# Optimization experiments

Measured on AMD Instinct MI355X. Metric: run time of the kernel, lower is better.

Reference implementation:

```python
import jax, jax.numpy as jnp
import numpy as np

B, T, D, H = 128, 1024, 256, 256


def setup_inputs() -> dict:
    key = jax.random.key(0)
    k1, k2, k3 = jax.random.split(key, 3)
    x = jax.random.normal(k1, (B, T, D), dtype=jnp.float32)
    # flax LSTMCell: input projections (no bias), hidden projections (with bias)
    Wi = jax.random.normal(k2, (D, 4 * H), dtype=jnp.float32) * (1.0 / np.sqrt(D))
    Wh = jax.random.normal(k3, (H, 4 * H), dtype=jnp.float32) * (1.0 / np.sqrt(H))
    bh = jnp.zeros((4 * H,), dtype=jnp.float32)
    return {"x": x, "Wi": Wi, "Wh": Wh, "bh": bh}


def reference(x, Wi, Wh, bh):
    # Unrolled LSTM over time with zero-initialized carry; dropout is identity
    # (deterministic, training=False).
    b, t, d = x.shape
    h_dim = Wh.shape[0]
    # Precompute all input-side gate projections: [B, T, 4H]
    xg = jnp.einsum("btd,dg->btg", x, Wi)

    def step(carry, xg_t):
        c, h = carry
        gates = xg_t + h @ Wh + bh  # [B, 4H]
        i, f, g, o = jnp.split(gates, 4, axis=-1)
        i = jax.nn.sigmoid(i)
        f = jax.nn.sigmoid(f)
        g = jnp.tanh(g)
        o = jax.nn.sigmoid(o)
        c_new = f * c + i * g
        h_new = o * jnp.tanh(c_new)
        return (c_new, h_new), h_new

    c0 = jnp.zeros((b, h_dim), dtype=x.dtype)
    h0 = jnp.zeros((b, h_dim), dtype=x.dtype)
    (c_fin, h_fin), ys = jax.lax.scan(step, (c0, h0), jnp.swapaxes(xg, 0, 1))
    outputs = jnp.swapaxes(ys, 0, 1)  # [B, T, H]
    return outputs, c_fin, h_fin
```

## Files before the change

kernel.cpp:

```cpp
#include <hip/hip_runtime.h>
#include <hip/hip_bf16.h>
#include <stdint.h>

typedef unsigned short u16;
typedef short short8 __attribute__((ext_vector_type(8)));
typedef float floatx4 __attribute__((ext_vector_type(4)));
typedef float f32x4 __attribute__((ext_vector_type(4)));

__device__ __forceinline__ u16 f2bf(float f) {
  union { float f; uint32_t u; } v; v.f = f;
  return (u16)((v.u + 0x7FFFu + ((v.u >> 16) & 1u)) >> 16);
}
__device__ __forceinline__ float fexp(float x) {
  return __builtin_amdgcn_exp2f(x * 1.44269504088896340736f);
}
__device__ __forceinline__ float sigm(float x) {
  return __builtin_amdgcn_rcpf(1.0f + fexp(-x));
}
__device__ __forceinline__ float tanh_(float x) {
  return 1.0f - 2.0f * __builtin_amdgcn_rcpf(1.0f + fexp(2.0f * x));
}
__device__ __forceinline__ uint32_t packbf(float hi, float lo) {
  union { float f; uint32_t u; } a, b; a.f = hi; b.f = lo;
  return __builtin_amdgcn_perm(a.u + 0x8000u, b.u + 0x8000u, 0x07060302u);
}

__device__ __forceinline__ short8 ld_b128_mall(const void* p) {
  short8 v;
  asm volatile("global_load_dwordx4 %0, %1, off sc0 sc1"
               : "=v"(v) : "v"(p) : "memory");
  return v;
}
__device__ __forceinline__ short8 ld_b128_xcd(const void* p) {
  short8 v;
  asm volatile("global_load_dwordx4 %0, %1, off sc0"
               : "=v"(v) : "v"(p) : "memory");
  return v;
}
__device__ __forceinline__ uint32_t ld_b32_mall_wait(const void* p) {
  uint32_t v;
  asm volatile("global_load_dword %0, %1, off sc0 sc1\n\ts_waitcnt vmcnt(0)"
               : "=v"(v) : "v"(p) : "memory");
  return v;
}
__device__ __forceinline__ uint32_t ld_b32_xcd_wait(const void* p) {
  uint32_t v;
  asm volatile("global_load_dword %0, %1, off sc0\n\ts_waitcnt vmcnt(0)"
               : "=v"(v) : "v"(p) : "memory");
  return v;
}
__device__ __forceinline__ void st_b16_mall(void* p, uint32_t v) {
  asm volatile("global_store_short %0, %1, off sc0 sc1"
               :: "v"(p), "v"(v) : "memory");
}
__device__ __forceinline__ void st_b32_mall(void* p, uint32_t v) {
  asm volatile("global_store_dword %0, %1, off sc0 sc1"
               :: "v"(p), "v"(v) : "memory");
}

__global__ void k1_prep(const float* __restrict__ Wi, const float* __restrict__ Wh,
                        u16* __restrict__ Wi_t, u16* __restrict__ Wh_t) {
  const int idx = blockIdx.x * 256 + threadIdx.x;
  const int n = idx >> 8, k = idx & 255;
  Wi_t[idx] = f2bf(Wi[k * 1024 + n]);
  Wh_t[idx] = f2bf(Wh[k * 1024 + n]);
}

template <bool FAST>
__device__ __forceinline__ void lstm_scan(
    const u16* __restrict__ Wi_t, const u16* __restrict__ Wh_t,
    const float* __restrict__ x, const float* __restrict__ bh,
    u16* __restrict__ h_ring, uint32_t* __restrict__ flags,
    float* __restrict__ out, int g, int j, int l) {
  const int lq = l >> 4, ln = l & 15;
  const int colBase = j * 16 + ln;

  short8 bfI[4][8], bfW[4][8];
#pragma unroll
  for (int gp = 0; gp < 4; ++gp)
#pragma unroll
    for (int kk = 0; kk < 8; ++kk) {
      const size_t o = (size_t)(gp * 256 + colBase) * 256 + kk * 32 + lq * 8;
      bfI[gp][kk] = *(const short8*)(Wi_t + o);
      bfW[gp][kk] = *(const short8*)(Wh_t + o);
    }
  float bias[4];
#pragma unroll
  for (int gp = 0; gp < 4; ++gp) bias[gp] = bh[gp * 256 + colBase];

  floatx4 xga[4];
  {
    f32x4 xf[16];
    const float* xp = x + (size_t)(g * 16 + ln) * 262144 + lq * 8;
#pragma unroll
    for (int kk = 0; kk < 8; ++kk) {
      xf[2 * kk]     = *(const f32x4*)(xp + kk * 32);
      xf[2 * kk + 1] = *(const f32x4*)(xp + kk * 32 + 4);
    }
#pragma unroll
    for (int gp = 0; gp < 4; ++gp)
      xga[gp] = (floatx4){bias[gp], bias[gp], bias[gp], bias[gp]};
#pragma unroll
    for (int kk = 0; kk < 8; ++kk) {
      union { uint32_t u[4]; short8 s; } cv;
      cv.u[0] = packbf(xf[2 * kk][1], xf[2 * kk][0]);
      cv.u[1] = packbf(xf[2 * kk][3], xf[2 * kk][2]);
      cv.u[2] = packbf(xf[2 * kk + 1][1], xf[2 * kk + 1][0]);
      cv.u[3] = packbf(xf[2 * kk + 1][3], xf[2 * kk + 1][2]);
#pragma unroll
      for (int gp = 0; gp < 4; ++gp)
        xga[gp] = __builtin_amdgcn_mfma_f32_16x16x32_bf16(cv.s, bfI[gp][kk],
                                                          xga[gp], 0, 0, 0);
    }
  }

  float creg[4] = {0.f, 0.f, 0.f, 0.f};
  float hv[4]   = {0.f, 0.f, 0.f, 0.f};

  for (int t = 0; t < 1024; ++t) {
    if (t > 0) {
      const uint32_t* fp = flags + (((g << 2) | (t & 3)) << 4) + (l & 15);
      if (FAST) { while (!__all(ld_b32_xcd_wait(fp)  == (uint32_t)t)) {} }
      else      { while (!__all(ld_b32_mall_wait(fp) == (uint32_t)t)) {} }
    }
    const u16* hs = h_ring + (size_t)(t & 3) * 32768 + g * 4096;
    short8 af[8];
#pragma unroll
    for (int kk = 0; kk < 8; ++kk) {
      const u16* ap = hs + ln * 256 + kk * 32 + lq * 8;
      af[kk] = FAST ? ld_b128_xcd(ap) : ld_b128_mall(ap);
    }
    f32x4 xf[16];
    if (t < 1023) {
      const float* xp = x + (size_t)(g * 16 + ln) * 262144 + (size_t)(t + 1) * 256 + lq * 8;
#pragma unroll
      for (int kk = 0; kk < 8; ++kk) {
        xf[2 * kk]     = *(const f32x4*)(xp + kk * 32);
        xf[2 * kk + 1] = *(const f32x4*)(xp + kk * 32 + 4);
      }
      asm volatile("s_waitcnt vmcnt(16)" ::: "memory");
    } else {
      asm volatile("s_waitcnt vmcnt(0)" ::: "memory");
    }
    __builtin_amdgcn_sched_barrier(0);
    floatx4 acc[4];
#pragma unroll
    for (int gp = 0; gp < 4; ++gp) acc[gp] = xga[gp];
#pragma unroll
    for (int kk = 0; kk < 8; ++kk)
#pragma unroll
      for (int gp = 0; gp < 4; ++gp)
        acc[gp] = __builtin_amdgcn_mfma_f32_16x16x32_bf16(af[kk], bfW[gp][kk],
                                                          acc[gp], 0, 0, 0);
#pragma unroll
    for (int r = 0; r < 4; ++r) {
      const float iv = sigm(acc[0][r]);
      const float fv = sigm(acc[1][r]);
      const float gv = tanh_(acc[2][r]);
      const float ov = sigm(acc[3][r]);
      const float cc = fv * creg[r] + iv * gv;
      creg[r] = cc;
      hv[r] = ov * tanh_(cc);
    }
    u16* hd = h_ring + (size_t)((t + 1) & 3) * 32768 + g * 4096;
#pragma unroll
    for (int r = 0; r < 4; ++r) {
      if (FAST) hd[(lq * 4 + r) * 256 + colBase] = f2bf(hv[r]);
      else st_b16_mall(hd + (lq * 4 + r) * 256 + colBase, (uint32_t)f2bf(hv[r]));
    }
    asm volatile("s_waitcnt vmcnt(0)" ::: "memory");
    if (l == 0) {
      uint32_t* fp = flags + (((g << 2) | ((t + 1) & 3)) << 4) + j;
      if (FAST) *fp = (uint32_t)(t + 1);
      else st_b32_mall(fp, (uint32_t)(t + 1));
    }
#pragma unroll
    for (int r = 0; r < 4; ++r) {
      float* yp = out + ((size_t)(g * 16 + lq * 4 + r) * 1024 + t) * 256 + colBase;
      if (FAST) *yp = hv[r];
      else __builtin_nontemporal_store(hv[r], yp);
    }
    if (t < 1023) {
#pragma unroll
      for (int gp = 0; gp < 4; ++gp)
        xga[gp] = (floatx4){bias[gp], bias[gp], bias[gp], bias[gp]};
#pragma unroll
      for (int kk = 0; kk < 8; ++kk) {
        union { uint32_t u[4]; short8 s; } cv;
        cv.u[0] = packbf(xf[2 * kk][1], xf[2 * kk][0]);
        cv.u[1] = packbf(xf[2 * kk][3], xf[2 * kk][2]);
        cv.u[2] = packbf(xf[2 * kk + 1][1], xf[2 * kk + 1][0]);
        cv.u[3] = packbf(xf[2 * kk + 1][3], xf[2 * kk + 1][2]);
#pragma unroll
        for (int gp = 0; gp < 4; ++gp)
          xga[gp] = __builtin_amdgcn_mfma_f32_16x16x32_bf16(cv.s, bfI[gp][kk],
                                                            xga[gp], 0, 0, 0);
      }
    }
  }
#pragma unroll
  for (int r = 0; r < 4; ++r) {
    const int b = g * 16 + lq * 4 + r;
    out[33554432 + b * 256 + colBase] = creg[r];
    out[33554432 + 32768 + b * 256 + colBase] = hv[r];
  }
}

__global__ __launch_bounds__(64, 1) void k3_lstm(
    const u16* __restrict__ Wi_t, const u16* __restrict__ Wh_t,
    const float* __restrict__ x, const float* __restrict__ bh,
    u16* __restrict__ h_ring, uint32_t* __restrict__ flags,
    uint32_t* __restrict__ xcc_arr, float* __restrict__ out) {
  const int g = blockIdx.x & 7;
  const int j = blockIdx.x >> 3;
  const int l = threadIdx.x;

  uint32_t xcc;
  asm volatile("s_getreg_b32 %0, hwreg(HW_REG_XCC_ID)" : "=s"(xcc));
  if (l == 0) st_b32_mall(xcc_arr + blockIdx.x, xcc + 1u);
  const uint32_t* xp_ = xcc_arr + g + 8 * (l & 15);
  uint32_t peer;
  do { peer = ld_b32_mall_wait(xp_); } while (!__all(peer != 0u));
  const bool fast = (bool)__all(peer == __builtin_amdgcn_readfirstlane(peer));

  if (fast) lstm_scan<true >(Wi_t, Wh_t, x, bh, h_ring, flags, out, g, j, l);
  else      lstm_scan<false>(Wi_t, Wh_t, x, bh, h_ring, flags, out, g, j, l);
}

extern "C" void kernel_launch(void* const* d_in, const int* in_sizes, int n_in,
                              void* d_out, int out_size, void* d_ws, size_t ws_size,
                              hipStream_t stream) {
  const float* x  = (const float*)d_in[0];
  const float* Wi = (const float*)d_in[1];
  const float* Wh = (const float*)d_in[2];
  const float* bh = (const float*)d_in[3];
  char* ws = (char*)d_ws;
  u16* Wi_t         = (u16*)(ws);
  u16* Wh_t         = (u16*)(ws + 524288);
  uint32_t* flags   = (uint32_t*)(ws + 1048576);
  uint32_t* xcc_arr = (uint32_t*)(ws + 1048576 + 2048);
  u16* h_ring       = (u16*)(ws + 1052672);
  float* out = (float*)d_out;

  hipMemsetAsync(ws + 1048576, 0, 4096, stream);
  hipMemsetAsync(h_ring, 0, 4 * 65536, stream);
  k1_prep<<<dim3(1024), dim3(256), 0, stream>>>(Wi, Wh, Wi_t, Wh_t);
  k3_lstm<<<dim3(128), dim3(64), 0, stream>>>(Wi_t, Wh_t, x, bh, h_ring, flags,
                                              xcc_arr, out);
}
```

Before: 2.603 ms.

## Prefetch x two steps ahead and pad flags to separate cache lines

The x loads for step t+2 are now issued after the current step's input projection is packed, so each load has a whole recurrence step to land. This lets the per-step wait become a full vmcnt(0) without stalling on fresh x loads. Each per-block sync flag is also padded to its own 64-byte slot, meant to stop false sharing and contention between the 16 flags polled per group. The flag, xcc and h_ring workspace offsets and the memset size grow to fit, at the cost of more registers for the packed bf16 operands.

```diff
diff --git a/kernel.cpp b/kernel.cpp
--- a/kernel.cpp
+++ b/kernel.cpp
@@ -88,30 +88,37 @@
 #pragma unroll
   for (int gp = 0; gp < 4; ++gp) bias[gp] = bh[gp * 256 + colBase];
 
+  const float* xrow = x + (size_t)(g * 16 + ln) * 262144 + lq * 8;
+  union CV { uint32_t u[4]; short8 s; };
+
+  f32x4 xf[16];
+  CV cv[8];
   floatx4 xga[4];
-  {
-    f32x4 xf[16];
-    const float* xp = x + (size_t)(g * 16 + ln) * 262144 + lq * 8;
-#pragma unroll
-    for (int kk = 0; kk < 8; ++kk) {
-      xf[2 * kk]     = *(const f32x4*)(xp + kk * 32);
-      xf[2 * kk + 1] = *(const f32x4*)(xp + kk * 32 + 4);
-    }
+#pragma unroll
+  for (int kk = 0; kk < 8; ++kk) {
+    xf[2 * kk]     = *(const f32x4*)(xrow + kk * 32);
+    xf[2 * kk + 1] = *(const f32x4*)(xrow + kk * 32 + 4);
+  }
+#pragma unroll
+  for (int kk = 0; kk < 8; ++kk) {
+    cv[kk].u[0] = packbf(xf[2 * kk][1], xf[2 * kk][0]);
+    cv[kk].u[1] = packbf(xf[2 * kk][3], xf[2 * kk][2]);
+    cv[kk].u[2] = packbf(xf[2 * kk + 1][1], xf[2 * kk + 1][0]);
+    cv[kk].u[3] = packbf(xf[2 * kk + 1][3], xf[2 * kk + 1][2]);
+  }
+#pragma unroll
+  for (int gp = 0; gp < 4; ++gp)
+    xga[gp] = (floatx4){bias[gp], bias[gp], bias[gp], bias[gp]};
+#pragma unroll
+  for (int kk = 0; kk < 8; ++kk)
 #pragma unroll
     for (int gp = 0; gp < 4; ++gp)
-      xga[gp] = (floatx4){bias[gp], bias[gp], bias[gp], bias[gp]};
-#pragma unroll
-    for (int kk = 0; kk < 8; ++kk) {
-      union { uint32_t u[4]; short8 s; } cv;
-      cv.u[0] = packbf(xf[2 * kk][1], xf[2 * kk][0]);
-      cv.u[1] = packbf(xf[2 * kk][3], xf[2 * kk][2]);
-      cv.u[2] = packbf(xf[2 * kk + 1][1], xf[2 * kk + 1][0]);
-      cv.u[3] = packbf(xf[2 * kk + 1][3], xf[2 * kk + 1][2]);
-#pragma unroll
-      for (int gp = 0; gp < 4; ++gp)
-        xga[gp] = __builtin_amdgcn_mfma_f32_16x16x32_bf16(cv.s, bfI[gp][kk],
-                                                          xga[gp], 0, 0, 0);
-    }
+      xga[gp] = __builtin_amdgcn_mfma_f32_16x16x32_bf16(cv[kk].s, bfI[gp][kk],
+                                                        xga[gp], 0, 0, 0);
+#pragma unroll
+  for (int kk = 0; kk < 8; ++kk) {
+    xf[2 * kk]     = *(const f32x4*)(xrow + 256 + kk * 32);
+    xf[2 * kk + 1] = *(const f32x4*)(xrow + 256 + kk * 32 + 4);
   }
 
   float creg[4] = {0.f, 0.f, 0.f, 0.f};
@@ -119,7 +126,7 @@
 
   for (int t = 0; t < 1024; ++t) {
     if (t > 0) {
-      const uint32_t* fp = flags + (((g << 2) | (t & 3)) << 4) + (l & 15);
+      const uint32_t* fp = flags + (((g << 2) | (t & 3)) << 8) + ((l & 15) << 4);
       if (FAST) { while (!__all(ld_b32_xcd_wait(fp)  == (uint32_t)t)) {} }
       else      { while (!__all(ld_b32_mall_wait(fp) == (uint32_t)t)) {} }
     }
@@ -130,18 +137,7 @@
       const u16* ap = hs + ln * 256 + kk * 32 + lq * 8;
       af[kk] = FAST ? ld_b128_xcd(ap) : ld_b128_mall(ap);
     }
-    f32x4 xf[16];
-    if (t < 1023) {
-      const float* xp = x + (size_t)(g * 16 + ln) * 262144 + (size_t)(t + 1) * 256 + lq * 8;
-#pragma unroll
-      for (int kk = 0; kk < 8; ++kk) {
-        xf[2 * kk]     = *(const f32x4*)(xp + kk * 32);
-        xf[2 * kk + 1] = *(const f32x4*)(xp + kk * 32 + 4);
-      }
-      asm volatile("s_waitcnt vmcnt(16)" ::: "memory");
-    } else {
-      asm volatile("s_waitcnt vmcnt(0)" ::: "memory");
-    }
+    asm volatile("s_waitcnt vmcnt(0)" ::: "memory");
     __builtin_amdgcn_sched_barrier(0);
     floatx4 acc[4];
 #pragma unroll
@@ -170,7 +166,7 @@
     }
     asm volatile("s_waitcnt vmcnt(0)" ::: "memory");
     if (l == 0) {
-      uint32_t* fp = flags + (((g << 2) | ((t + 1) & 3)) << 4) + j;
+      uint32_t* fp = flags + (((g << 2) | ((t + 1) & 3)) << 8) + (j << 4);
       if (FAST) *fp = (uint32_t)(t + 1);
       else st_b32_mall(fp, (uint32_t)(t + 1));
     }
@@ -182,20 +178,29 @@
     }
     if (t < 1023) {
 #pragma unroll
+      for (int kk = 0; kk < 8; ++kk) {
+        cv[kk].u[0] = packbf(xf[2 * kk][1], xf[2 * kk][0]);
+        cv[kk].u[1] = packbf(xf[2 * kk][3], xf[2 * kk][2]);
+        cv[kk].u[2] = packbf(xf[2 * kk + 1][1], xf[2 * kk + 1][0]);
+        cv[kk].u[3] = packbf(xf[2 * kk + 1][3], xf[2 * kk + 1][2]);
+      }
+      if (t < 1022) {
+        const float* xp = xrow + (size_t)(t + 2) * 256;
+#pragma unroll
+        for (int kk = 0; kk < 8; ++kk) {
+          xf[2 * kk]     = *(const f32x4*)(xp + kk * 32);
+          xf[2 * kk + 1] = *(const f32x4*)(xp + kk * 32 + 4);
+        }
+      }
+#pragma unroll
       for (int gp = 0; gp < 4; ++gp)
         xga[gp] = (floatx4){bias[gp], bias[gp], bias[gp], bias[gp]};
 #pragma unroll
-      for (int kk = 0; kk < 8; ++kk) {
-        union { uint32_t u[4]; short8 s; } cv;
-        cv.u[0] = packbf(xf[2 * kk][1], xf[2 * kk][0]);
-        cv.u[1] = packbf(xf[2 * kk][3], xf[2 * kk][2]);
-        cv.u[2] = packbf(xf[2 * kk + 1][1], xf[2 * kk + 1][0]);
-        cv.u[3] = packbf(xf[2 * kk + 1][3], xf[2 * kk + 1][2]);
+      for (int kk = 0; kk < 8; ++kk)
 #pragma unroll
         for (int gp = 0; gp < 4; ++gp)
-          xga[gp] = __builtin_amdgcn_mfma_f32_16x16x32_bf16(cv.s, bfI[gp][kk],
+          xga[gp] = __builtin_amdgcn_mfma_f32_16x16x32_bf16(cv[kk].s, bfI[gp][kk],
                                                             xga[gp], 0, 0, 0);
-      }
     }
   }
 #pragma unroll
@@ -238,11 +243,11 @@
   u16* Wi_t         = (u16*)(ws);
   u16* Wh_t         = (u16*)(ws + 524288);
   uint32_t* flags   = (uint32_t*)(ws + 1048576);
-  uint32_t* xcc_arr = (uint32_t*)(ws + 1048576 + 2048);
-  u16* h_ring       = (u16*)(ws + 1052672);
+  uint32_t* xcc_arr = (uint32_t*)(ws + 1048576 + 32768);
+  u16* h_ring       = (u16*)(ws + 1048576 + 36864);
   float* out = (float*)d_out;
 
-  hipMemsetAsync(ws + 1048576, 0, 4096, stream);
+  hipMemsetAsync(ws + 1048576, 0, 36864, stream);
   hipMemsetAsync(h_ring, 0, 4 * 65536, stream);
   k1_prep<<<dim3(1024), dim3(256), 0, stream>>>(Wi, Wh, Wi_t, Wh_t);
   k3_lstm<<<dim3(128), dim3(64), 0, stream>>>(Wi_t, Wh_t, x, bh, h_ring, flags,
```

Result: no change. 2.602 ms (-0.0%).
